# Performance work log

Measured on AMD Instinct MI355X. Metric: run time of the kernel, lower is better.

The kernel has to match this reference:

```python
import jax, jax.numpy as jnp
import numpy as np

N = 100000        # num nodes
E = 1600000       # num edges (before self-loops)
F_IN = 128        # num_node_features
HEADS = 8
HID = 8           # per-head hidden channels in conv1 (hardcoded in module)
C = 16            # num_classes
NEG_SLOPE = 0.2   # PyG GATConv default


def setup_inputs() -> dict:
    key = jax.random.key(0)
    ks = jax.random.split(key, 10)
    x = jax.random.normal(ks[0], (N, F_IN), jnp.float32)
    edge_index = jax.random.randint(ks[1], (2, E), 0, N, dtype=jnp.int32)
    s1 = 1.0 / np.sqrt(F_IN)
    s2 = 1.0 / np.sqrt(HEADS * HID)
    W1 = jax.random.normal(ks[2], (F_IN, HEADS * HID), jnp.float32) * s1
    att_src1 = jax.random.normal(ks[3], (HEADS, HID), jnp.float32) * s1
    att_dst1 = jax.random.normal(ks[4], (HEADS, HID), jnp.float32) * s1
    b1 = jnp.zeros((HEADS * HID,), jnp.float32)
    W2 = jax.random.normal(ks[5], (HEADS * HID, C), jnp.float32) * s2
    att_src2 = jax.random.normal(ks[6], (1, C), jnp.float32) * s2
    att_dst2 = jax.random.normal(ks[7], (1, C), jnp.float32) * s2
    b2 = jnp.zeros((C,), jnp.float32)
    return {"x": x, "edge_index": edge_index, "W1": W1, "att_src1": att_src1,
            "att_dst1": att_dst1, "b1": b1, "W2": W2, "att_src2": att_src2,
            "att_dst2": att_dst2, "b2": b2}


def gat_conv(x, edge_index, W, att_src, att_dst, bias, heads, out_ch, concat):
    """PyG-style GATConv (eval mode; add_self_loops=True)."""
    n = x.shape[0]
    loop = jnp.arange(n, dtype=edge_index.dtype)
    src = jnp.concatenate([edge_index[0], loop])   # message source j
    dst = jnp.concatenate([edge_index[1], loop])   # message target i
    h = (x @ W).reshape(n, heads, out_ch)          # [N, H, O]
    a_s = jnp.einsum('nho,ho->nh', h, att_src)     # [N, H]
    a_d = jnp.einsum('nho,ho->nh', h, att_dst)
    e = jax.nn.leaky_relu(a_s[src] + a_d[dst], NEG_SLOPE)     # [E', H]
    m = jax.lax.stop_gradient(jax.ops.segment_max(e, dst, num_segments=n))
    ex = jnp.exp(e - m[dst])
    denom = jax.ops.segment_sum(ex, dst, num_segments=n)      # [N, H]
    alpha = ex / (denom[dst] + 1e-16)                         # [E', H]
    out = jax.ops.segment_sum(h[src] * alpha[:, :, None], dst, num_segments=n)
    out = out.reshape(n, heads * out_ch) if concat else out.mean(axis=1)
    return out + bias


def reference(x, edge_index, W1, att_src1, att_dst1, b1, W2, att_src2, att_dst2, b2):
    h = gat_conv(x, edge_index, W1, att_src1, att_dst1, b1, HEADS, HID, True)
    h = jax.nn.relu(h)  # dropout is identity in eval mode
    out = gat_conv(h, edge_index, W2, att_src2, att_dst2, b2, 1, C, False)
    return jax.nn.log_softmax(out, axis=1)
```

## Files before the change

### kernel.cpp

```cpp
#include <hip/hip_runtime.h>
#include <hip/hip_bf16.h>

#define NN 100000
#define FIN 128
#define H8 64
#define NC 16
#define BKS 9
#define BMASK 511
#define CHUNK 8192

typedef unsigned short ushort_t;
typedef unsigned int uint_t;

__device__ __forceinline__ float bu2f(ushort_t u) {
    unsigned v = ((unsigned)u) << 16;
    return __uint_as_float(v);
}
__device__ __forceinline__ ushort_t f2bu(float f) {
    __hip_bfloat16 h = __float2bfloat16(f);
    return *reinterpret_cast<ushort_t*>(&h);
}
__device__ __forceinline__ float dot4(float4 a, float4 b) {
    return a.x * b.x + a.y * b.y + a.z * b.z + a.w * b.w;
}
__device__ __forceinline__ void fma4(float4& a, float s, float4 w) {
    a.x += s * w.x; a.y += s * w.y; a.z += s * w.z; a.w += s * w.w;
}


__global__ __launch_bounds__(256) void k_binA(const int* __restrict__ dst,
        int* __restrict__ bh, int e, int nb, int nblk) {
    __shared__ int hist[256];
    int t = threadIdx.x;
    hist[t] = 0;
    __syncthreads();
    int base = blockIdx.x * CHUNK;
    int endj = min(base + CHUNK, e);
    for (int k0 = base + t * 4; k0 < endj; k0 += 1024) {
        if (k0 + 3 < endj) {
            int4 d4 = *(const int4*)(dst + k0);
            atomicAdd(&hist[d4.x >> BKS], 1);
            atomicAdd(&hist[d4.y >> BKS], 1);
            atomicAdd(&hist[d4.z >> BKS], 1);
            atomicAdd(&hist[d4.w >> BKS], 1);
        } else {
            for (int k = k0; k < endj; ++k) atomicAdd(&hist[dst[k] >> BKS], 1);
        }
    }
    __syncthreads();
    if (t < nb) bh[t * nblk + blockIdx.x] = hist[t];
}

__global__ __launch_bounds__(256) void k_scanB(int* __restrict__ bh,
        int* __restrict__ btot, int nblk) {
    __shared__ int ts[256];
    int j = blockIdx.x, t = threadIdx.x;
    int v = (t < nblk) ? bh[j * nblk + t] : 0;
    ts[t] = v;
    __syncthreads();
    int run = v;
    for (int off = 1; off < 256; off <<= 1) {
        int y = (t >= off) ? ts[t - off] : 0;
        __syncthreads();
        run += y;
        ts[t] = run;
        __syncthreads();
    }
    if (t < nblk) bh[j * nblk + t] = run - v;
    if (t == 255) btot[j] = run;
}

__global__ __launch_bounds__(256) void k_scanT(const int* __restrict__ btot,
        int* __restrict__ bstart, int nb) {
    __shared__ int ts[256];
    int j = threadIdx.x;
    int s = (j < nb) ? btot[j] : 0;
    ts[j] = s;
    __syncthreads();
    int run = s;
    for (int off = 1; off < 256; off <<= 1) {
        int y = (j >= off) ? ts[j - off] : 0;
        __syncthreads();
        run += y;
        ts[j] = run;
        __syncthreads();
    }
    if (j < nb) bstart[j] = run - s;
    if (j == nb - 1) bstart[nb] = run;
}

__global__ __launch_bounds__(256) void k_binC(const int* __restrict__ src,
        const int* __restrict__ dst, const int* __restrict__ bh,
        const int* __restrict__ bstart, uint_t* __restrict__ binned,
        int e, int nb, int nblk) {
    __shared__ int off[256];
    int t = threadIdx.x;
    if (t < nb) off[t] = bh[t * nblk + blockIdx.x] + bstart[t];
    __syncthreads();
    int base = blockIdx.x * CHUNK;
    int endj = min(base + CHUNK, e);
    for (int k0 = base + t * 4; k0 < endj; k0 += 1024) {
        if (k0 + 3 < endj) {
            int4 d4 = *(const int4*)(dst + k0);
            int4 s4 = *(const int4*)(src + k0);
            int p0 = atomicAdd(&off[d4.x >> BKS], 1);
            binned[p0] = ((uint_t)(d4.x & BMASK) << 17) | (uint_t)s4.x;
            int p1 = atomicAdd(&off[d4.y >> BKS], 1);
            binned[p1] = ((uint_t)(d4.y & BMASK) << 17) | (uint_t)s4.y;
            int p2 = atomicAdd(&off[d4.z >> BKS], 1);
            binned[p2] = ((uint_t)(d4.z & BMASK) << 17) | (uint_t)s4.z;
            int p3 = atomicAdd(&off[d4.w >> BKS], 1);
            binned[p3] = ((uint_t)(d4.w & BMASK) << 17) | (uint_t)s4.w;
        } else {
            for (int k = k0; k < endj; ++k) {
                int d = dst[k], s = src[k];
                int p = atomicAdd(&off[d >> BKS], 1);
                binned[p] = ((uint_t)(d & BMASK) << 17) | (uint_t)s;
            }
        }
    }
}

__global__ __launch_bounds__(256) void k_bucket(const uint_t* __restrict__ binned,
        const int* __restrict__ bstart, int* __restrict__ rp, int* __restrict__ col,
        int e, int n, int nb) {
    __shared__ int deg[512];
    __shared__ int ts[256];
    int b = blockIdx.x, t = threadIdx.x;
    int node0 = b << BKS;
    int S = bstart[b];
    int Se = bstart[b + 1];
    deg[t] = 0; deg[t + 256] = 0;
    __syncthreads();
    for (int k = S + t; k < Se; k += 256)
        atomicAdd(&deg[binned[k] >> 17], 1);
    __syncthreads();
    int g0 = node0 + 2 * t, g1 = g0 + 1;
    int c0 = (g0 < n) ? deg[2 * t] + 1 : 0;
    int c1 = (g1 < n) ? deg[2 * t + 1] + 1 : 0;
    int s = c0 + c1;
    ts[t] = s;
    __syncthreads();
    int run = s;
    for (int off = 1; off < 256; off <<= 1) {
        int y = (t >= off) ? ts[t - off] : 0;
        __syncthreads();
        run += y;
        ts[t] = run;
        __syncthreads();
    }
    int ex = run - s;
    int base = S + node0;
    int p0 = base + ex, p1 = base + ex + c0;
    if (g0 < n) { rp[g0] = p0; col[p0] = g0; deg[2 * t] = p0 + 1; }
    if (g1 < n) { rp[g1] = p1; col[p1] = g1; deg[2 * t + 1] = p1 + 1; }
    if (b == nb - 1 && t == 0) rp[n] = e + n;
    __syncthreads();
    for (int k = S + t; k < Se; k += 256) {
        uint_t pk = binned[k];
        int dLow = pk >> 17;
        int sv = (int)(pk & 0x1FFFFu);
        int p = atomicAdd(&deg[dLow], 1);
        col[p] = sv;
    }
}


__global__ __launch_bounds__(256) void k_gemm1(const float* __restrict__ x,
        const float* __restrict__ W, const float* __restrict__ attS,
        const float* __restrict__ attD, ushort_t* __restrict__ h1b,
        float* __restrict__ as1, float* __restrict__ ad1, int n) {
    __shared__ float ws[FIN * H8];
    int t = threadIdx.x;
    const float4* W4 = (const float4*)W;
    float4* ws4 = (float4*)ws;
    for (int j = t; j < FIN * H8 / 4; j += 256) ws4[j] = W4[j];
    __syncthreads();

    int wv = t >> 6, lane = t & 63;
    int ng = lane >> 4, cg = lane & 15;
    int node0 = (blockIdx.x * 4 + wv) * 16 + ng * 4;

    int r0 = min(node0 + 0, n - 1), r1 = min(node0 + 1, n - 1);
    int r2 = min(node0 + 2, n - 1), r3 = min(node0 + 3, n - 1);
    const float* xp0 = x + (long)r0 * FIN;
    const float* xp1 = x + (long)r1 * FIN;
    const float* xp2 = x + (long)r2 * FIN;
    const float* xp3 = x + (long)r3 * FIN;

    float4 a0 = {0, 0, 0, 0}, a1 = {0, 0, 0, 0}, a2 = {0, 0, 0, 0}, a3 = {0, 0, 0, 0};
#pragma unroll 2
    for (int k = 0; k < FIN; k += 4) {
        float4 xa = *(const float4*)(xp0 + k);
        float4 xb = *(const float4*)(xp1 + k);
        float4 xc = *(const float4*)(xp2 + k);
        float4 xd = *(const float4*)(xp3 + k);
        float4 w0 = *(const float4*)(ws + (k + 0) * H8 + cg * 4);
        float4 w1 = *(const float4*)(ws + (k + 1) * H8 + cg * 4);
        float4 w2 = *(const float4*)(ws + (k + 2) * H8 + cg * 4);
        float4 w3 = *(const float4*)(ws + (k + 3) * H8 + cg * 4);
        fma4(a0, xa.x, w0); fma4(a0, xa.y, w1); fma4(a0, xa.z, w2); fma4(a0, xa.w, w3);
        fma4(a1, xb.x, w0); fma4(a1, xb.y, w1); fma4(a1, xb.z, w2); fma4(a1, xb.w, w3);
        fma4(a2, xc.x, w0); fma4(a2, xc.y, w1); fma4(a2, xc.z, w2); fma4(a2, xc.w, w3);
        fma4(a3, xd.x, w0); fma4(a3, xd.y, w1); fma4(a3, xd.z, w2); fma4(a3, xd.w, w3);
    }

    float4 sA = *(const float4*)(attS + cg * 4);
    float4 dA = *(const float4*)(attD + cg * 4);
    float4 av[4] = {a0, a1, a2, a3};
#pragma unroll
    for (int j = 0; j < 4; ++j) {
        int node = node0 + j;
        float4 a = av[j];
        float vs = dot4(a, sA);
        float vd = dot4(a, dA);
        vs += __shfl_xor(vs, 1, 64);
        vd += __shfl_xor(vd, 1, 64);
        if (node < n) {
            ushort4 q;
            q.x = f2bu(a.x); q.y = f2bu(a.y); q.z = f2bu(a.z); q.w = f2bu(a.w);
            *(ushort4*)(h1b + (long)node * H8 + cg * 4) = q;
            if ((lane & 1) == 0) {
                as1[node * 8 + (cg >> 1)] = vs;
                ad1[node * 8 + (cg >> 1)] = vd;
            }
        }
    }
}


__global__ __launch_bounds__(256) void k_agg1(const int* __restrict__ rp,
        const int* __restrict__ col, const ushort_t* __restrict__ h1b,
        const float* __restrict__ as1, const float* __restrict__ ad1,
        const float* __restrict__ b1, ushort_t* __restrict__ z1b, int n) {
    int w = (blockIdx.x * 256 + threadIdx.x) >> 6;
    int lane = threadIdx.x & 63;
    int iA = w * 2, iB = iA + 1;
    if (iA >= n) return;
    bool hasB = (iB < n);
    int slot = lane >> 3;
    int h2 = lane & 7;
    int l16 = lane & 15;
    int begA = rp[iA], endA = rp[iA + 1];
    int begB = hasB ? rp[iB] : 0, endB = hasB ? rp[iB + 1] : 0;
    int lastA = endA - 1, lastB = endB - 1;
    float adiA = ad1[iA * 8 + h2];
    float adiB = hasB ? ad1[iB * 8 + h2] : 0.f;
    float denA = 0.f, denB = 0.f;
    float numA[8] = {0.f, 0.f, 0.f, 0.f, 0.f, 0.f, 0.f, 0.f};
    float numB[8] = {0.f, 0.f, 0.f, 0.f, 0.f, 0.f, 0.f, 0.f};
    int roundsA = (endA - begA + 15) >> 4;
    int roundsB = hasB ? ((endB - begB + 15) >> 4) : 0;
    int rmax = max(roundsA, roundsB);
    int vA = col[min(begA + l16, lastA)];
    int vB = roundsB ? col[min(begB + l16, lastB)] : 0;
    for (int r = 0; r < rmax; ++r) {
        bool mA = r < roundsA, mB = r < roundsB;
        int kA0 = begA + r * 16, kB0 = begB + r * 16;
        int vnA = 0, vnB = 0;
        if (r + 1 < roundsA) vnA = col[min(kA0 + 16 + l16, lastA)];
        if (r + 1 < roundsB) vnB = col[min(kB0 + 16 + l16, lastB)];
        float pAa = 0.f, pAb = 0.f, pBa = 0.f, pBb = 0.f;
        uint4 uaA, ubA, uaB, ubB;
        if (mA) {
            int s0 = __shfl(vA, slot, 64);
            int s1 = __shfl(vA, 8 + slot, 64);
            float sv0 = as1[s0 * 8 + h2];
            float sv1 = as1[s1 * 8 + h2];
            uaA = *((const uint4*)(h1b + ((size_t)(unsigned)s0 << 6)) + h2);
            ubA = *((const uint4*)(h1b + ((size_t)(unsigned)s1 << 6)) + h2);
            float e0 = sv0 + adiA;
            e0 = fmaxf(e0, 0.f) + 0.2f * fminf(e0, 0.f);
            pAa = (kA0 + slot < endA) ? __expf(e0) : 0.f;
            float e1 = sv1 + adiA;
            e1 = fmaxf(e1, 0.f) + 0.2f * fminf(e1, 0.f);
            pAb = (kA0 + 8 + slot < endA) ? __expf(e1) : 0.f;
            denA += pAa + pAb;
        }
        if (mB) {
            int s0 = __shfl(vB, slot, 64);
            int s1 = __shfl(vB, 8 + slot, 64);
            float sv0 = as1[s0 * 8 + h2];
            float sv1 = as1[s1 * 8 + h2];
            uaB = *((const uint4*)(h1b + ((size_t)(unsigned)s0 << 6)) + h2);
            ubB = *((const uint4*)(h1b + ((size_t)(unsigned)s1 << 6)) + h2);
            float e0 = sv0 + adiB;
            e0 = fmaxf(e0, 0.f) + 0.2f * fminf(e0, 0.f);
            pBa = (kB0 + slot < endB) ? __expf(e0) : 0.f;
            float e1 = sv1 + adiB;
            e1 = fmaxf(e1, 0.f) + 0.2f * fminf(e1, 0.f);
            pBb = (kB0 + 8 + slot < endB) ? __expf(e1) : 0.f;
            denB += pBa + pBb;
        }
#define ACC8(NUM, P, U)                                                    \
        {                                                                  \
            NUM[0] += (P) * __uint_as_float((U).x << 16);                  \
            NUM[1] += (P) * __uint_as_float((U).x & 0xffff0000u);          \
            NUM[2] += (P) * __uint_as_float((U).y << 16);                  \
            NUM[3] += (P) * __uint_as_float((U).y & 0xffff0000u);          \
            NUM[4] += (P) * __uint_as_float((U).z << 16);                  \
            NUM[5] += (P) * __uint_as_float((U).z & 0xffff0000u);          \
            NUM[6] += (P) * __uint_as_float((U).w << 16);                  \
            NUM[7] += (P) * __uint_as_float((U).w & 0xffff0000u);          \
        }
        if (mA) { ACC8(numA, pAa, uaA) ACC8(numA, pAb, ubA) }
        if (mB) { ACC8(numB, pBa, uaB) ACC8(numB, pBb, ubB) }
#undef ACC8
        vA = vnA; vB = vnB;
    }
#pragma unroll
    for (int q = 0; q < 8; ++q) {
        numA[q] += __shfl_xor(numA[q], 8, 64);
        numA[q] += __shfl_xor(numA[q], 16, 64);
        numA[q] += __shfl_xor(numA[q], 32, 64);
        numB[q] += __shfl_xor(numB[q], 8, 64);
        numB[q] += __shfl_xor(numB[q], 16, 64);
        numB[q] += __shfl_xor(numB[q], 32, 64);
    }
    denA += __shfl_xor(denA, 8, 64);
    denA += __shfl_xor(denA, 16, 64);
    denA += __shfl_xor(denA, 32, 64);
    denB += __shfl_xor(denB, 8, 64);
    denB += __shfl_xor(denB, 16, 64);
    denB += __shfl_xor(denB, 32, 64);
    if (lane < 16) {
        bool isB = lane >= 8;
        if (!isB || hasB) {
            int node = isB ? iB : iA;
            const float* nm = isB ? numB : numA;
            float invd = 1.0f / ((isB ? denB : denA) + 1e-16f);
            float4 b0 = *(const float4*)(b1 + h2 * 8);
            float4 b1v = *(const float4*)(b1 + h2 * 8 + 4);
            float o0 = fmaxf(nm[0] * invd + b0.x, 0.f);
            float o1 = fmaxf(nm[1] * invd + b0.y, 0.f);
            float o2 = fmaxf(nm[2] * invd + b0.z, 0.f);
            float o3 = fmaxf(nm[3] * invd + b0.w, 0.f);
            float o4 = fmaxf(nm[4] * invd + b1v.x, 0.f);
            float o5 = fmaxf(nm[5] * invd + b1v.y, 0.f);
            float o6 = fmaxf(nm[6] * invd + b1v.z, 0.f);
            float o7 = fmaxf(nm[7] * invd + b1v.w, 0.f);
            uint4 q;
            q.x = (uint_t)f2bu(o0) | ((uint_t)f2bu(o1) << 16);
            q.y = (uint_t)f2bu(o2) | ((uint_t)f2bu(o3) << 16);
            q.z = (uint_t)f2bu(o4) | ((uint_t)f2bu(o5) << 16);
            q.w = (uint_t)f2bu(o6) | ((uint_t)f2bu(o7) << 16);
            *(uint4*)(z1b + (size_t)node * H8 + h2 * 8) = q;
        }
    }
}


__global__ __launch_bounds__(256) void k_gemm2(const ushort_t* __restrict__ z1b,
        const float* __restrict__ W2, const float* __restrict__ attS,
        const float* __restrict__ attD, ushort_t* __restrict__ h2b,
        float* __restrict__ as2, float* __restrict__ ad2) {
    __shared__ float ws[H8 * NC];
    __shared__ float zs[16][H8 + 1];
    int t = threadIdx.x;
    for (int j = t; j < H8 * NC; j += 256) ws[j] = W2[j];
    int n0 = blockIdx.x * 16;
    {
        const ushort4* zp = (const ushort4*)(z1b + (size_t)n0 * H8);
        ushort4 q = zp[t];
        int r = t >> 4, k2 = (t & 15) * 4;
        zs[r][k2 + 0] = bu2f(q.x);
        zs[r][k2 + 1] = bu2f(q.y);
        zs[r][k2 + 2] = bu2f(q.z);
        zs[r][k2 + 3] = bu2f(q.w);
    }
    __syncthreads();
    int c = t & 15, g = t >> 4;
    float acc = 0.f;
#pragma unroll 8
    for (int k = 0; k < H8; ++k) acc += zs[g][k] * ws[k * NC + c];
    h2b[(long)(n0 + g) * NC + c] = f2bu(acc);
    float vs = acc * attS[c], vd = acc * attD[c];
    for (int off = 1; off < 16; off <<= 1) {
        vs += __shfl_xor(vs, off, 64);
        vd += __shfl_xor(vd, off, 64);
    }
    if (c == 0) { as2[n0 + g] = vs; ad2[n0 + g] = vd; }
}


__global__ __launch_bounds__(256) void k_agg2(const int* __restrict__ rp,
        const int* __restrict__ col, const ushort_t* __restrict__ h2b,
        const float* __restrict__ as2, const float* __restrict__ ad2,
        const float* __restrict__ b2, float* __restrict__ out, int n) {
    int i = (blockIdx.x * 256 + threadIdx.x) >> 6;
    int lane = threadIdx.x & 63;
    if (i >= n) return;
    int grp = lane >> 3;
    int cp = lane & 7;
    int beg = rp[i], end = rp[i + 1];
    int last = end - 1;
    int deg = end - beg;
    float adi = ad2[i];
    const uint_t* h2u = (const uint_t*)h2b;
    float denp = 0.f, nx = 0.f, ny = 0.f;
    int rounds = (deg + 31) >> 5;
    for (int r = 0; r < rounds; ++r) {
        int k = beg + r * 32;
        int rem = end - k;
        int v = col[min(k + (lane & 31), last)];
        float sv = as2[v];
        float e = sv + adi;
        e = fmaxf(e, 0.f) + 0.2f * fminf(e, 0.f);
        int lim = min(rem, 32);
        float p = (lane < lim) ? __expf(e) : 0.f;
        denp += p;
#define AGG2_PAIR(S0, S1)                                                  \
        {                                                                  \
            int i0 = (S0) * 8 + grp, i1 = (S1) * 8 + grp;                  \
            int r0 = __shfl(v, i0, 64), r1 = __shfl(v, i1, 64);            \
            float q0 = __shfl(p, i0, 64), q1 = __shfl(p, i1, 64);          \
            uint_t u0 = h2u[((size_t)(unsigned)r0 << 3) + cp];             \
            uint_t u1 = h2u[((size_t)(unsigned)r1 << 3) + cp];             \
            nx += q0 * __uint_as_float(u0 << 16);                          \
            ny += q0 * __uint_as_float(u0 & 0xffff0000u);                  \
            nx += q1 * __uint_as_float(u1 << 16);                          \
            ny += q1 * __uint_as_float(u1 & 0xffff0000u);                  \
        }
        AGG2_PAIR(0, 1)
        if (lim > 16) AGG2_PAIR(2, 3)
#undef AGG2_PAIR
    }
    nx += __shfl_xor(nx, 8, 64);  ny += __shfl_xor(ny, 8, 64);
    nx += __shfl_xor(nx, 16, 64); ny += __shfl_xor(ny, 16, 64);
    nx += __shfl_xor(nx, 32, 64); ny += __shfl_xor(ny, 32, 64);
    denp += __shfl_xor(denp, 1, 64);
    denp += __shfl_xor(denp, 2, 64);
    denp += __shfl_xor(denp, 4, 64);
    denp += __shfl_xor(denp, 8, 64);
    denp += __shfl_xor(denp, 16, 64);
    denp += __shfl_xor(denp, 32, 64);
    float invd = 1.0f / (denp + 1e-16f);
    float2 bp = ((const float2*)b2)[cp];
    float ox = nx * invd + bp.x;
    float oy = ny * invd + bp.y;
    float mx = fmaxf(ox, oy);
    mx = fmaxf(mx, __shfl_xor(mx, 1, 64));
    mx = fmaxf(mx, __shfl_xor(mx, 2, 64));
    mx = fmaxf(mx, __shfl_xor(mx, 4, 64));
    float sm = __expf(ox - mx) + __expf(oy - mx);
    sm += __shfl_xor(sm, 1, 64);
    sm += __shfl_xor(sm, 2, 64);
    sm += __shfl_xor(sm, 4, 64);
    float lg = mx + __logf(sm);
    if (lane < 8) {
        float2 res = {ox - lg, oy - lg};
        ((float2*)(out + (size_t)i * NC))[cp] = res;
    }
}


extern "C" void kernel_launch(void* const* d_in, const int* in_sizes, int n_in,
                              void* d_out, int out_size, void* d_ws, size_t ws_size,
                              hipStream_t stream) {
    const float* x     = (const float*)d_in[0];
    const int*   ei    = (const int*)d_in[1];
    const float* W1    = (const float*)d_in[2];
    const float* attS1 = (const float*)d_in[3];
    const float* attD1 = (const float*)d_in[4];
    const float* b1    = (const float*)d_in[5];
    const float* W2    = (const float*)d_in[6];
    const float* attS2 = (const float*)d_in[7];
    const float* attD2 = (const float*)d_in[8];
    const float* b2    = (const float*)d_in[9];
    float* out = (float*)d_out;

    const int N = NN;
    const int E = in_sizes[1] / 2;
    const int NB = (N + (1 << BKS) - 1) >> BKS;
    const int NBLK = (E + CHUNK - 1) / CHUNK;

    ushort_t* z1b = (ushort_t*)d_ws;
    float* as1 = (float*)(z1b + (size_t)N * H8);
    float* ad1 = as1 + (size_t)N * 8;
    float* as2 = ad1 + (size_t)N * 8;
    float* ad2 = as2 + N;
    ushort_t* h1b = (ushort_t*)(ad2 + N);
    ushort_t* h2b = h1b + (size_t)N * H8;
    int* rp   = (int*)(h2b + (size_t)N * NC);
    int* col  = rp + (N + 1);
    int* bh   = col + (E + N);
    int* btot = bh + (size_t)NB * NBLK;
    int* bstart = btot + NB;
    uint_t* binned = (uint_t*)z1b;

    const int* srcp = ei;
    const int* dstp = ei + E;

    k_binA<<<NBLK, 256, 0, stream>>>(dstp, bh, E, NB, NBLK);
    k_scanB<<<NB, 256, 0, stream>>>(bh, btot, NBLK);
    k_scanT<<<1, 256, 0, stream>>>(btot, bstart, NB);
    k_binC<<<NBLK, 256, 0, stream>>>(srcp, dstp, bh, bstart, binned, E, NB, NBLK);
    k_bucket<<<NB, 256, 0, stream>>>(binned, bstart, rp, col, E, N, NB);

    k_gemm1<<<(N + 63) / 64, 256, 0, stream>>>(x, W1, attS1, attD1, h1b, as1, ad1, N);
    k_agg1<<<(N + 7) / 8, 256, 0, stream>>>(rp, col, h1b, as1, ad1, b1, z1b, N);
    k_gemm2<<<N / 16, 256, 0, stream>>>(z1b, W2, attS2, attD2, h2b, as2, ad2);
    k_agg2<<<(N + 3) / 4, 256, 0, stream>>>(rp, col, h2b, as2, ad2, b2, out, N);
}
```

Measured before the change: 180.2 us.

## Split gemm1 blocks across CSR-build kernels to overlap independent work

The first-layer GEMM is split into three parts, and each part is launched as extra blocks inside the histogram, scan and scatter kernels of the CSR build. The small, latency-bound binning kernels then share the GPU with independent GEMM work, and one kernel launch is removed. As a trade-off, every fused kernel now reserves 32KB of shared memory per block, which may lower occupancy for the binning blocks, and the GEMM blocks can delay the critical binning path.

```diff
diff --git a/kernel.cpp b/kernel.cpp
--- a/kernel.cpp
+++ b/kernel.cpp
@@ -28,13 +28,74 @@
 }
 
 
-__global__ __launch_bounds__(256) void k_binA(const int* __restrict__ dst,
-        int* __restrict__ bh, int e, int nb, int nblk) {
-    __shared__ int hist[256];
+__device__ __forceinline__ void gemm1_body(int gb,
+        const float* __restrict__ x, const float* __restrict__ W,
+        const float* __restrict__ attS, const float* __restrict__ attD,
+        ushort_t* __restrict__ h1b, float* __restrict__ as1,
+        float* __restrict__ ad1, int n, float* ws) {
+    int t = threadIdx.x;
+    const float4* W4 = (const float4*)W;
+    float4* ws4 = (float4*)ws;
+    for (int j = t; j < FIN * H8 / 4; j += 256) ws4[j] = W4[j];
+    __syncthreads();
+
+    int wv = t >> 6, lane = t & 63;
+    int ng = lane >> 4, cg = lane & 15;
+    int node0 = (gb * 4 + wv) * 16 + ng * 4;
+
+    int r0 = min(node0 + 0, n - 1), r1 = min(node0 + 1, n - 1);
+    int r2 = min(node0 + 2, n - 1), r3 = min(node0 + 3, n - 1);
+    const float* xp0 = x + (long)r0 * FIN;
+    const float* xp1 = x + (long)r1 * FIN;
+    const float* xp2 = x + (long)r2 * FIN;
+    const float* xp3 = x + (long)r3 * FIN;
+
+    float4 a0 = {0, 0, 0, 0}, a1 = {0, 0, 0, 0}, a2 = {0, 0, 0, 0}, a3 = {0, 0, 0, 0};
+#pragma unroll 2
+    for (int k = 0; k < FIN; k += 4) {
+        float4 xa = *(const float4*)(xp0 + k);
+        float4 xb = *(const float4*)(xp1 + k);
+        float4 xc = *(const float4*)(xp2 + k);
+        float4 xd = *(const float4*)(xp3 + k);
+        float4 w0 = *(const float4*)(ws + (k + 0) * H8 + cg * 4);
+        float4 w1 = *(const float4*)(ws + (k + 1) * H8 + cg * 4);
+        float4 w2 = *(const float4*)(ws + (k + 2) * H8 + cg * 4);
+        float4 w3 = *(const float4*)(ws + (k + 3) * H8 + cg * 4);
+        fma4(a0, xa.x, w0); fma4(a0, xa.y, w1); fma4(a0, xa.z, w2); fma4(a0, xa.w, w3);
+        fma4(a1, xb.x, w0); fma4(a1, xb.y, w1); fma4(a1, xb.z, w2); fma4(a1, xb.w, w3);
+        fma4(a2, xc.x, w0); fma4(a2, xc.y, w1); fma4(a2, xc.z, w2); fma4(a2, xc.w, w3);
+        fma4(a3, xd.x, w0); fma4(a3, xd.y, w1); fma4(a3, xd.z, w2); fma4(a3, xd.w, w3);
+    }
+
+    float4 sA = *(const float4*)(attS + cg * 4);
+    float4 dA = *(const float4*)(attD + cg * 4);
+    float4 av[4] = {a0, a1, a2, a3};
+#pragma unroll
+    for (int j = 0; j < 4; ++j) {
+        int node = node0 + j;
+        float4 a = av[j];
+        float vs = dot4(a, sA);
+        float vd = dot4(a, dA);
+        vs += __shfl_xor(vs, 1, 64);
+        vd += __shfl_xor(vd, 1, 64);
+        if (node < n) {
+            ushort4 q;
+            q.x = f2bu(a.x); q.y = f2bu(a.y); q.z = f2bu(a.z); q.w = f2bu(a.w);
+            *(ushort4*)(h1b + (long)node * H8 + cg * 4) = q;
+            if ((lane & 1) == 0) {
+                as1[node * 8 + (cg >> 1)] = vs;
+                ad1[node * 8 + (cg >> 1)] = vd;
+            }
+        }
+    }
+}
+
+__device__ __forceinline__ void binA_body(int cb, const int* __restrict__ dst,
+        int* __restrict__ bh, int e, int nb, int nblk, int* hist) {
     int t = threadIdx.x;
     hist[t] = 0;
     __syncthreads();
-    int base = blockIdx.x * CHUNK;
+    int base = cb * CHUNK;
     int endj = min(base + CHUNK, e);
     for (int k0 = base + t * 4; k0 < endj; k0 += 1024) {
         if (k0 + 3 < endj) {
@@ -48,13 +109,12 @@
         }
     }
     __syncthreads();
-    if (t < nb) bh[t * nblk + blockIdx.x] = hist[t];
-}
-
-__global__ __launch_bounds__(256) void k_scanB(int* __restrict__ bh,
-        int* __restrict__ btot, int nblk) {
-    __shared__ int ts[256];
-    int j = blockIdx.x, t = threadIdx.x;
+    if (t < nb) bh[t * nblk + cb] = hist[t];
+}
+
+__device__ __forceinline__ void scanB_body(int j, int* __restrict__ bh,
+        int* __restrict__ btot, int nblk, int* ts) {
+    int t = threadIdx.x;
     int v = (t < nblk) ? bh[j * nblk + t] : 0;
     ts[t] = v;
     __syncthreads();
@@ -70,34 +130,14 @@
     if (t == 255) btot[j] = run;
 }
 
-__global__ __launch_bounds__(256) void k_scanT(const int* __restrict__ btot,
-        int* __restrict__ bstart, int nb) {
-    __shared__ int ts[256];
-    int j = threadIdx.x;
-    int s = (j < nb) ? btot[j] : 0;
-    ts[j] = s;
-    __syncthreads();
-    int run = s;
-    for (int off = 1; off < 256; off <<= 1) {
-        int y = (j >= off) ? ts[j - off] : 0;
-        __syncthreads();
-        run += y;
-        ts[j] = run;
-        __syncthreads();
-    }
-    if (j < nb) bstart[j] = run - s;
-    if (j == nb - 1) bstart[nb] = run;
-}
-
-__global__ __launch_bounds__(256) void k_binC(const int* __restrict__ src,
+__device__ __forceinline__ void binC_body(int cb, const int* __restrict__ src,
         const int* __restrict__ dst, const int* __restrict__ bh,
         const int* __restrict__ bstart, uint_t* __restrict__ binned,
-        int e, int nb, int nblk) {
-    __shared__ int off[256];
+        int e, int nb, int nblk, int* off) {
     int t = threadIdx.x;
-    if (t < nb) off[t] = bh[t * nblk + blockIdx.x] + bstart[t];
-    __syncthreads();
-    int base = blockIdx.x * CHUNK;
+    if (t < nb) off[t] = bh[t * nblk + cb] + bstart[t];
+    __syncthreads();
+    int base = cb * CHUNK;
     int endj = min(base + CHUNK, e);
     for (int k0 = base + t * 4; k0 < endj; k0 += 1024) {
         if (k0 + 3 < endj) {
@@ -121,6 +161,67 @@
     }
 }
 
+
+__global__ __launch_bounds__(256) void k_fuseA(const int* __restrict__ dst,
+        int* __restrict__ bh, int e, int nb, int nblk,
+        const float* __restrict__ x, const float* __restrict__ W,
+        const float* __restrict__ attS, const float* __restrict__ attD,
+        ushort_t* __restrict__ h1b, float* __restrict__ as1,
+        float* __restrict__ ad1, int n) {
+    __shared__ float smem[FIN * H8];
+    if ((int)blockIdx.x < nblk)
+        binA_body(blockIdx.x, dst, bh, e, nb, nblk, (int*)smem);
+    else
+        gemm1_body(blockIdx.x - nblk, x, W, attS, attD, h1b, as1, ad1, n, smem);
+}
+
+__global__ __launch_bounds__(256) void k_fuseB(int* __restrict__ bh,
+        int* __restrict__ btot, int nblk, int nb, int g1ofs,
+        const float* __restrict__ x, const float* __restrict__ W,
+        const float* __restrict__ attS, const float* __restrict__ attD,
+        ushort_t* __restrict__ h1b, float* __restrict__ as1,
+        float* __restrict__ ad1, int n) {
+    __shared__ float smem[FIN * H8];
+    if ((int)blockIdx.x < nb)
+        scanB_body(blockIdx.x, bh, btot, nblk, (int*)smem);
+    else
+        gemm1_body(g1ofs + blockIdx.x - nb, x, W, attS, attD, h1b, as1, ad1, n, smem);
+}
+
+__global__ __launch_bounds__(256) void k_fuseC(const int* __restrict__ src,
+        const int* __restrict__ dst, const int* __restrict__ bh,
+        const int* __restrict__ bstart, uint_t* __restrict__ binned,
+        int e, int nb, int nblk, int g1ofs,
+        const float* __restrict__ x, const float* __restrict__ W,
+        const float* __restrict__ attS, const float* __restrict__ attD,
+        ushort_t* __restrict__ h1b, float* __restrict__ as1,
+        float* __restrict__ ad1, int n) {
+    __shared__ float smem[FIN * H8];
+    if ((int)blockIdx.x < nblk)
+        binC_body(blockIdx.x, src, dst, bh, bstart, binned, e, nb, nblk, (int*)smem);
+    else
+        gemm1_body(g1ofs + blockIdx.x - nblk, x, W, attS, attD, h1b, as1, ad1, n, smem);
+}
+
+__global__ __launch_bounds__(256) void k_scanT(const int* __restrict__ btot,
+        int* __restrict__ bstart, int nb) {
+    __shared__ int ts[256];
+    int j = threadIdx.x;
+    int s = (j < nb) ? btot[j] : 0;
+    ts[j] = s;
+    __syncthreads();
+    int run = s;
+    for (int off = 1; off < 256; off <<= 1) {
+        int y = (j >= off) ? ts[j - off] : 0;
+        __syncthreads();
+        run += y;
+        ts[j] = run;
+        __syncthreads();
+    }
+    if (j < nb) bstart[j] = run - s;
+    if (j == nb - 1) bstart[nb] = run;
+}
+
 __global__ __launch_bounds__(256) void k_bucket(const uint_t* __restrict__ binned,
         const int* __restrict__ bstart, int* __restrict__ rp, int* __restrict__ col,
         int e, int n, int nb) {
@@ -162,69 +263,6 @@
         int sv = (int)(pk & 0x1FFFFu);
         int p = atomicAdd(&deg[dLow], 1);
         col[p] = sv;
-    }
-}
-
-
-__global__ __launch_bounds__(256) void k_gemm1(const float* __restrict__ x,
-        const float* __restrict__ W, const float* __restrict__ attS,
-        const float* __restrict__ attD, ushort_t* __restrict__ h1b,
-        float* __restrict__ as1, float* __restrict__ ad1, int n) {
-    __shared__ float ws[FIN * H8];
-    int t = threadIdx.x;
-    const float4* W4 = (const float4*)W;
-    float4* ws4 = (float4*)ws;
-    for (int j = t; j < FIN * H8 / 4; j += 256) ws4[j] = W4[j];
-    __syncthreads();
-
-    int wv = t >> 6, lane = t & 63;
-    int ng = lane >> 4, cg = lane & 15;
-    int node0 = (blockIdx.x * 4 + wv) * 16 + ng * 4;
-
-    int r0 = min(node0 + 0, n - 1), r1 = min(node0 + 1, n - 1);
-    int r2 = min(node0 + 2, n - 1), r3 = min(node0 + 3, n - 1);
-    const float* xp0 = x + (long)r0 * FIN;
-    const float* xp1 = x + (long)r1 * FIN;
-    const float* xp2 = x + (long)r2 * FIN;
-    const float* xp3 = x + (long)r3 * FIN;
-
-    float4 a0 = {0, 0, 0, 0}, a1 = {0, 0, 0, 0}, a2 = {0, 0, 0, 0}, a3 = {0, 0, 0, 0};
-#pragma unroll 2
-    for (int k = 0; k < FIN; k += 4) {
-        float4 xa = *(const float4*)(xp0 + k);
-        float4 xb = *(const float4*)(xp1 + k);
-        float4 xc = *(const float4*)(xp2 + k);
-        float4 xd = *(const float4*)(xp3 + k);
-        float4 w0 = *(const float4*)(ws + (k + 0) * H8 + cg * 4);
-        float4 w1 = *(const float4*)(ws + (k + 1) * H8 + cg * 4);
-        float4 w2 = *(const float4*)(ws + (k + 2) * H8 + cg * 4);
-        float4 w3 = *(const float4*)(ws + (k + 3) * H8 + cg * 4);
-        fma4(a0, xa.x, w0); fma4(a0, xa.y, w1); fma4(a0, xa.z, w2); fma4(a0, xa.w, w3);
-        fma4(a1, xb.x, w0); fma4(a1, xb.y, w1); fma4(a1, xb.z, w2); fma4(a1, xb.w, w3);
-        fma4(a2, xc.x, w0); fma4(a2, xc.y, w1); fma4(a2, xc.z, w2); fma4(a2, xc.w, w3);
-        fma4(a3, xd.x, w0); fma4(a3, xd.y, w1); fma4(a3, xd.z, w2); fma4(a3, xd.w, w3);
-    }
-
-    float4 sA = *(const float4*)(attS + cg * 4);
-    float4 dA = *(const float4*)(attD + cg * 4);
-    float4 av[4] = {a0, a1, a2, a3};
-#pragma unroll
-    for (int j = 0; j < 4; ++j) {
-        int node = node0 + j;
-        float4 a = av[j];
-        float vs = dot4(a, sA);
-        float vd = dot4(a, dA);
-        vs += __shfl_xor(vs, 1, 64);
-        vd += __shfl_xor(vd, 1, 64);
-        if (node < n) {
-            ushort4 q;
-            q.x = f2bu(a.x); q.y = f2bu(a.y); q.z = f2bu(a.z); q.w = f2bu(a.w);
-            *(ushort4*)(h1b + (long)node * H8 + cg * 4) = q;
-            if ((lane & 1) == 0) {
-                as1[node * 8 + (cg >> 1)] = vs;
-                ad1[node * 8 + (cg >> 1)] = vd;
-            }
-        }
     }
 }
 
@@ -491,13 +529,20 @@
     const int* srcp = ei;
     const int* dstp = ei + E;
 
-    k_binA<<<NBLK, 256, 0, stream>>>(dstp, bh, E, NB, NBLK);
-    k_scanB<<<NB, 256, 0, stream>>>(bh, btot, NBLK);
+    const int G1 = (N + 63) / 64;
+    const int G1A = G1 * 1 / 3;
+    const int G1B = G1 * 1 / 3;
+    const int G1C = G1 - G1A - G1B;
+
+    k_fuseA<<<NBLK + G1A, 256, 0, stream>>>(dstp, bh, E, NB, NBLK,
+            x, W1, attS1, attD1, h1b, as1, ad1, N);
+    k_fuseB<<<NB + G1B, 256, 0, stream>>>(bh, btot, NBLK, NB, G1A,
+            x, W1, attS1, attD1, h1b, as1, ad1, N);
     k_scanT<<<1, 256, 0, stream>>>(btot, bstart, NB);
-    k_binC<<<NBLK, 256, 0, stream>>>(srcp, dstp, bh, bstart, binned, E, NB, NBLK);
+    k_fuseC<<<NBLK + G1C, 256, 0, stream>>>(srcp, dstp, bh, bstart, binned,
+            E, NB, NBLK, G1A + G1B, x, W1, attS1, attD1, h1b, as1, ad1, N);
     k_bucket<<<NB, 256, 0, stream>>>(binned, bstart, rp, col, E, N, NB);
 
-    k_gemm1<<<(N + 63) / 64, 256, 0, stream>>>(x, W1, attS1, attD1, h1b, as1, ad1, N);
     k_agg1<<<(N + 7) / 8, 256, 0, stream>>>(rp, col, h1b, as1, ad1, b1, z1b, N);
     k_gemm2<<<N / 16, 256, 0, stream>>>(z1b, W2, attS2, attD2, h2b, as2, ad2);
     k_agg2<<<(N + 3) / 4, 256, 0, stream>>>(rp, col, h2b, as2, ad2, b2, out, N);
```

After: 179.5 us (median of 2 runs). Within noise of the previous version (-0.4%).
